# Performance work log

Hardware: AMD Instinct MI355X
Metric: run time of the kernel (lower is better)

The kernel has to match this reference:

```python
import jax, jax.numpy as jnp
import numpy as np

B, T, IN, H, OUT = 256, 100, 128, 1024, 35
BITS = 4
SLOPE = 25.0
THR_H = 1.0
THR_O = 1.0
BETA1, BETA2, BETA3, BETA4 = 0.9, 0.85, 0.8, 0.95


def fake_quant(w, w_min, w_max, bits=BITS):
    # FakeQuantize in training mode: STE -> forward value is quantized, grad passes through clamp
    levels = 2 ** bits
    scale = (w_max - w_min) / (levels - 1)
    wc = jnp.clip(w, w_min, w_max)
    q = jnp.round((wc - w_min) / scale) * scale + w_min
    return wc + jax.lax.stop_gradient(q - wc)


@jax.custom_vjp
def spike(x):
    # Heaviside forward, fast-sigmoid surrogate backward (snn.surrogate.fast_sigmoid)
    return (x > 0).astype(x.dtype)

def _spike_fwd(x):
    return (x > 0).astype(x.dtype), x

def _spike_bwd(x, g):
    return (g / (SLOPE * jnp.abs(x) + 1.0) ** 2,)

spike.defvjp(_spike_fwd, _spike_bwd)


def lif_step(cur, mem, beta, thr, reset_mechanism):
    # snntorch Leaky (reset_delay semantics): reset computed from previous mem, detached
    reset = jax.lax.stop_gradient((mem > thr).astype(cur.dtype))
    base = beta * mem + cur
    if reset_mechanism == "subtract":
        mem_new = base - reset * thr
    else:  # "zero"
        mem_new = base - reset * base
    spk = spike(mem_new - thr)
    return spk, mem_new


def setup_inputs() -> dict:
    key = jax.random.key(0)
    ks = jax.random.split(key, 5)
    x = jax.random.normal(ks[0], (B, T, IN), dtype=jnp.float32)
    # QuantLinear init: uniform(w_min, w_max); fc1 uses (-0.5, 0.5), others (0.001, 1.0)
    w1 = jax.random.uniform(ks[1], (H, IN), minval=-0.5, maxval=0.5, dtype=jnp.float32)
    w2 = jax.random.uniform(ks[2], (H, H), minval=0.001, maxval=1.0, dtype=jnp.float32)
    w3 = jax.random.uniform(ks[3], (H, H), minval=0.001, maxval=1.0, dtype=jnp.float32)
    w4 = jax.random.uniform(ks[4], (OUT, H), minval=0.001, maxval=1.0, dtype=jnp.float32)
    return {"x": x, "w1": w1, "w2": w2, "w3": w3, "w4": w4}


def reference(x, w1, w2, w3, w4):
    # hoist weight quantization out of the time loop (identical math each step)
    q1 = fake_quant(w1, -0.5, 0.5)
    q2 = fake_quant(w2, 0.001, 1.0)
    q3 = fake_quant(w3, 0.001, 1.0)
    q4 = fake_quant(w4, 0.001, 1.0)
    xs = jnp.transpose(x, (1, 0, 2)) / 15.0  # [T, B, IN]
    Bx = x.shape[0]

    def step(carry, xt):
        m1, m2, m3, m4 = carry
        s1, m1 = lif_step(xt @ q1.T, m1, BETA1, THR_H, "subtract")
        s2, m2 = lif_step(s1 @ q2.T, m2, BETA2, THR_H, "subtract")
        s3, m3 = lif_step(s2 @ q3.T, m3, BETA3, THR_H, "subtract")
        s4, m4 = lif_step(s3 @ q4.T, m4, BETA4, THR_O, "zero")
        return (m1, m2, m3, m4), (s1, s2, s3, s4, m4)

    init = (jnp.zeros((Bx, H), x.dtype), jnp.zeros((Bx, H), x.dtype),
            jnp.zeros((Bx, H), x.dtype), jnp.zeros((Bx, OUT), x.dtype))
    _, (spk1, spk2, spk3, spk4, mem4) = jax.lax.scan(step, init, xs)
    # stacked along time dim 0, matching torch.stack(dim=0)
    return spk1, spk2, spk3, spk4, mem4
```

## Files before the change

### kernel.cpp

```cpp
#include <hip/hip_runtime.h>
#include <stdint.h>

#define NB  256
#define NT  100
#define NIN 128
#define NH  1024
#define NOUT 35
#define NR  25600

#define O_SPK2 26214400ull
#define O_SPK3 52428800ull
#define O_SPK4 78643200ull
#define O_MEM4 79539200ull

#define WS_KBUF 0ull
#define WS_SPKB 52428800ull
#define WS_K2B  78643200ull
#define WS_K3B  79691776ull
#define WS_K4B  80740352ull
#define WS_Q1T  80871424ull
#define WS_N1   81395712ull
#define WS_N2   81498112ull
#define WS_N3   81600512ull

#define S2C ((float)((1.0 - 0.001) / 15.0))
#define S1C ((float)(1.0 / 15.0))

typedef int v4i __attribute__((ext_vector_type(4)));

__device__ __forceinline__ void async16(const void* g, void* l) {
  __builtin_amdgcn_global_load_lds((const __attribute__((address_space(1))) uint32_t*)g,
                                   (__attribute__((address_space(3))) uint32_t*)l, 16, 0, 0);
}

__device__ __forceinline__ uint8_t qk(float w) {
  float wc = fminf(fmaxf(w, 0.001f), 1.0f);
  return (uint8_t)(int)rintf((wc - 0.001f) / S2C);
}

__global__ void k_prep(const float* __restrict__ w1, const float* __restrict__ w2,
                       const float* __restrict__ w3, const float* __restrict__ w4,
                       uint8_t* __restrict__ ws)
{
  long long id = (long long)blockIdx.x * 256 + threadIdx.x;
  if (id < 1048576) { ws[WS_K2B + id] = qk(w2[id]); return; }
  id -= 1048576;
  if (id < 1048576) { ws[WS_K3B + id] = qk(w3[id]); return; }
  id -= 1048576;
  if (id < 131072) {
    int j = (int)(id >> 10), i = (int)(id & 1023);
    ws[WS_K4B + id] = (j < NOUT) ? qk(w4[(size_t)j * 1024 + i]) : (uint8_t)0;
    return;
  }
  id -= 131072;
  if (id < 131072) {
    int i = (int)(id >> 10), j = (int)(id & 1023);
    float wv = w1[(size_t)j * 128 + i];
    float wc = fminf(fmaxf(wv, -0.5f), 0.5f);
    float q = rintf((wc + 0.5f) / S1C) * S1C - 0.5f;
    ((float*)(ws + WS_Q1T))[id] = q;
    return;
  }
  id -= 131072;
  if (id < 76800) ((uint32_t*)(ws + WS_N1))[id] = 0;
}

__global__ __launch_bounds__(256) void k_cur1(const float* __restrict__ x,
                                              const uint8_t* __restrict__ ws,
                                              float* __restrict__ out)
{
  __shared__ float xsT[128 * 68];
  __shared__ float qch[16 * 256];
  const float* q1T = (const float*)(ws + WS_Q1T);
  const int tid = threadIdx.x;
  const int rb = blockIdx.x >> 2, cb = blockIdx.x & 3;
  const int t = rb >> 2, b0 = (rb & 3) * 64;
  const int jI = tid & 63, rI = tid >> 6;
  const int j4 = jI * 4, r16 = rI * 16;

  #pragma unroll
  for (int k = 0; k < 32; ++k) {
    int e = tid + k * 256;
    int r = e >> 7, i = e & 127;
    xsT[i * 68 + r] = x[((size_t)(b0 + r) * NT + t) * NIN + i] / 15.0f;
  }
  float acc[16][4];
  #pragma unroll
  for (int d = 0; d < 16; ++d) { acc[d][0]=0.f; acc[d][1]=0.f; acc[d][2]=0.f; acc[d][3]=0.f; }
  for (int ic = 0; ic < 8; ++ic) {
    __syncthreads();
    #pragma unroll
    for (int k = 0; k < 16; ++k) {
      int e = tid + k * 256;
      int ii = e >> 8, j = e & 255;
      qch[ii * 256 + j] = q1T[((size_t)(ic * 16 + ii) << 10) + cb * 256 + j];
    }
    __syncthreads();
    #pragma unroll
    for (int ii = 0; ii < 16; ++ii) {
      int i = ic * 16 + ii;
      const float4 q  = *(const float4*)&qch[ii * 256 + j4];
      const float4 xa = *(const float4*)&xsT[i * 68 + r16];
      const float4 xb = *(const float4*)&xsT[i * 68 + r16 + 4];
      const float4 xc = *(const float4*)&xsT[i * 68 + r16 + 8];
      const float4 xd = *(const float4*)&xsT[i * 68 + r16 + 12];
      float xr[16];
      xr[0]=xa.x; xr[1]=xa.y; xr[2]=xa.z; xr[3]=xa.w;
      xr[4]=xb.x; xr[5]=xb.y; xr[6]=xb.z; xr[7]=xb.w;
      xr[8]=xc.x; xr[9]=xc.y; xr[10]=xc.z; xr[11]=xc.w;
      xr[12]=xd.x; xr[13]=xd.y; xr[14]=xd.z; xr[15]=xd.w;
      #pragma unroll
      for (int d = 0; d < 16; ++d) {
        acc[d][0] = fmaf(xr[d], q.x, acc[d][0]);
        acc[d][1] = fmaf(xr[d], q.y, acc[d][1]);
        acc[d][2] = fmaf(xr[d], q.z, acc[d][2]);
        acc[d][3] = fmaf(xr[d], q.w, acc[d][3]);
      }
    }
  }
  #pragma unroll
  for (int d = 0; d < 16; ++d) {
    float4 v = make_float4(acc[d][0], acc[d][1], acc[d][2], acc[d][3]);
    *(float4*)&out[((size_t)rb * 64 + r16 + d) * 1024 + cb * 256 + j4] = v;
  }
}

__global__ __launch_bounds__(256) void k_scan1(uint8_t* __restrict__ ws, float* __restrict__ out)
{
  const int tid = threadIdx.x;
  const int b = blockIdx.x >> 2;
  const int j = (blockIdx.x & 3) * 256 + tid;
  uint8_t* spkb = ws + WS_SPKB;
  uint32_t* n1 = (uint32_t*)(ws + WS_N1);
  const size_t stride = (size_t)NB * NH;
  size_t idx = (size_t)b * NH + j;
  float m = 0.f;
  float c = out[idx];
  for (int t = 0; t < NT; ++t) {
    float cn = (t + 1 < NT) ? out[idx + stride] : 0.f;
    float rst = m > 1.0f ? 1.0f : 0.0f;
    m = fmaf(0.9f, m, c) - rst;
    bool sp = (m - 1.0f) > 0.0f;
    out[idx] = sp ? 1.0f : 0.0f;
    spkb[idx] = sp ? 1 : 0;
    unsigned long long bal = __ballot(sp);
    if ((tid & 63) == 0) atomicAdd((unsigned int*)&n1[t * NB + b], (unsigned)__popcll(bal));
    idx += stride; c = cn;
  }
}

__global__ __launch_bounds__(256) void k_gemm(const uint8_t* __restrict__ A,
                                              const uint8_t* __restrict__ Bm,
                                              uint16_t* __restrict__ C, int ncb)
{
  __shared__ uint8_t sA[16384];
  __shared__ uint8_t sB[16384];
  const int tid = threadIdx.x, lane = tid & 63, wave = tid >> 6;
  const int lm = lane & 15, lk = lane >> 4;
  const int rb = blockIdx.x, jb = blockIdx.y;
  const int mw = wave & 1, nw = wave >> 1;
  v4i acc[4][4];
  #pragma unroll
  for (int a = 0; a < 4; ++a)
    #pragma unroll
    for (int bb = 0; bb < 4; ++bb) { acc[a][bb][0]=0; acc[a][bb][1]=0; acc[a][bb][2]=0; acc[a][bb][3]=0; }

  for (int kk = 0; kk < 1024; kk += 128) {
    __syncthreads();
    #pragma unroll
    for (int q = 0; q < 8; ++q) {
      int cid = wave * 8 + q;
      if (cid < 16) {
        int kh = cid >> 3, cm = cid & 7;
        const uint8_t* g = A + (size_t)(rb * 128 + cm * 16 + lm) * 1024 + kk + kh * 64 + (lk << 4);
        async16(g, sA + cid * 1024);
      } else {
        int cb2 = cid - 16;
        int kh = cb2 >> 3, cn = cb2 & 7;
        const uint8_t* g = Bm + (size_t)(jb * 128 + cn * 16 + lm) * 1024 + kk + kh * 64 + (lk << 4);
        async16(g, sB + cb2 * 1024);
      }
    }
    __syncthreads();
    #pragma unroll
    for (int kh = 0; kh < 2; ++kh) {
      v4i av[4], bv[4];
      #pragma unroll
      for (int mi = 0; mi < 4; ++mi)
        av[mi] = *(const v4i*)(sA + (size_t)(kh * 8 + mw * 4 + mi) * 1024 + lane * 16);
      #pragma unroll
      for (int ni = 0; ni < 4; ++ni)
        bv[ni] = *(const v4i*)(sB + (size_t)(kh * 8 + nw * 4 + ni) * 1024 + lane * 16);
      #pragma unroll
      for (int mi = 0; mi < 4; ++mi)
        #pragma unroll
        for (int ni = 0; ni < 4; ++ni)
          acc[mi][ni] = __builtin_amdgcn_mfma_i32_16x16x64_i8(av[mi], bv[ni], acc[mi][ni], 0, 0, 0);
    }
  }
  const int rowb = rb * 128 + mw * 64;
  const int colb = jb * 128 + nw * 64;
  const int strideC = ncb * 128;
  #pragma unroll
  for (int mi = 0; mi < 4; ++mi)
    #pragma unroll
    for (int ni = 0; ni < 4; ++ni)
      #pragma unroll
      for (int r = 0; r < 4; ++r) {
        int row = rowb + mi * 16 + (lane >> 4) * 4 + r;
        int col = colb + ni * 16 + (lane & 15);
        C[(size_t)row * strideC + col] = (uint16_t)acc[mi][ni][r];
      }
}

__global__ __launch_bounds__(256) void k_scan23(const uint16_t* __restrict__ Kin,
                                                const uint32_t* __restrict__ nprev,
                                                uint32_t* __restrict__ nout,
                                                float beta,
                                                float* __restrict__ outB,
                                                uint8_t* __restrict__ spkb)
{
  const int tid = threadIdx.x;
  const int b = blockIdx.x >> 2;
  const int j = (blockIdx.x & 3) * 256 + tid;
  const size_t stride = (size_t)NB * NH;
  size_t idx = (size_t)b * NH + j;
  float m = 0.f;
  uint16_t kv = Kin[idx];
  for (int t = 0; t < NT; ++t) {
    uint16_t kn = (t + 1 < NT) ? Kin[idx + stride] : (uint16_t)0;
    float nb = 0.001f * (float)nprev[t * NB + b];
    float cur = fmaf(S2C, (float)kv, nb);
    float rst = m > 1.0f ? 1.0f : 0.0f;
    m = fmaf(beta, m, cur) - rst;
    bool sp = (m - 1.0f) > 0.0f;
    outB[idx] = sp ? 1.0f : 0.0f;
    spkb[idx] = sp ? 1 : 0;
    unsigned long long bal = __ballot(sp);
    if ((tid & 63) == 0) atomicAdd((unsigned int*)&nout[t * NB + b], (unsigned)__popcll(bal));
    idx += stride; kv = kn;
  }
}

__global__ __launch_bounds__(64) void k_scan4(const uint8_t* __restrict__ ws, float* __restrict__ out)
{
  const int b = blockIdx.x;
  const int j = threadIdx.x;
  const uint16_t* K4 = (const uint16_t*)(ws + WS_KBUF);
  const uint32_t* n3 = (const uint32_t*)(ws + WS_N3);
  size_t idx = (size_t)b * 128 + j;
  const size_t stride = (size_t)NB * 128;
  float m = 0.f;
  uint16_t kv = (j < NOUT) ? K4[idx] : (uint16_t)0;
  for (int t = 0; t < NT; ++t) {
    uint16_t kn = (t + 1 < NT && j < NOUT) ? K4[idx + stride] : (uint16_t)0;
    float cur = fmaf(S2C, (float)kv, 0.001f * (float)n3[t * NB + b]);
    float rst = m > 1.0f ? 1.0f : 0.0f;
    float bsv = fmaf(0.95f, m, cur);
    m = (rst > 0.0f) ? 0.0f : bsv;
    if (j < NOUT) {
      size_t rowO = ((size_t)t * NB + b) * NOUT + j;
      out[O_SPK4 + rowO] = ((m - 1.0f) > 0.0f) ? 1.0f : 0.0f;
      out[O_MEM4 + rowO] = m;
    }
    idx += stride; kv = kn;
  }
}

extern "C" void kernel_launch(void* const* d_in, const int* in_sizes, int n_in,
                              void* d_out, int out_size, void* d_ws, size_t ws_size,
                              hipStream_t stream)
{
  const float* x  = (const float*)d_in[0];
  const float* w1 = (const float*)d_in[1];
  const float* w2 = (const float*)d_in[2];
  const float* w3 = (const float*)d_in[3];
  const float* w4 = (const float*)d_in[4];
  float* out = (float*)d_out;
  uint8_t* ws = (uint8_t*)d_ws;

  uint16_t* KBUF = (uint16_t*)(ws + WS_KBUF);
  uint8_t*  SPKB = ws + WS_SPKB;
  uint32_t* N1 = (uint32_t*)(ws + WS_N1);
  uint32_t* N2 = (uint32_t*)(ws + WS_N2);
  uint32_t* N3 = (uint32_t*)(ws + WS_N3);

  hipLaunchKernelGGL(k_prep, dim3(9517), dim3(256), 0, stream, w1, w2, w3, w4, ws);
  hipLaunchKernelGGL(k_cur1, dim3(1600), dim3(256), 0, stream, x, ws, out);
  hipLaunchKernelGGL(k_scan1, dim3(1024), dim3(256), 0, stream, ws, out);
  hipLaunchKernelGGL(k_gemm, dim3(200, 8), dim3(256), 0, stream, SPKB, ws + WS_K2B, KBUF, 8);
  hipLaunchKernelGGL(k_scan23, dim3(1024), dim3(256), 0, stream, KBUF, N1, N2, 0.85f, out + O_SPK2, SPKB);
  hipLaunchKernelGGL(k_gemm, dim3(200, 8), dim3(256), 0, stream, SPKB, ws + WS_K3B, KBUF, 8);
  hipLaunchKernelGGL(k_scan23, dim3(1024), dim3(256), 0, stream, KBUF, N2, N3, 0.8f, out + O_SPK3, SPKB);
  hipLaunchKernelGGL(k_gemm, dim3(200, 1), dim3(256), 0, stream, SPKB, ws + WS_K4B, KBUF, 1);
  hipLaunchKernelGGL(k_scan4, dim3(256), dim3(64), 0, stream, ws, out);
}
```

Before: 747.2 us.

## Fuse per-layer GEMM with LIF time scan using per-batch tiles over time

Each layer's matmul and its time-recurrent LIF scan now run in one kernel. Blocks tile over (batch, 128 output columns), and the M dimension is the 100 timesteps padded to 112. The GEMM result stays in LDS and a single thread per column scans it over time. This removes the intermediate uint16 current buffer round trip through global memory and cuts the launch count. In exchange, only 128 threads per block do the serial scan, and padded rows add some wasted MFMA work.

```diff
diff --git a/kernel.cpp b/kernel.cpp
--- a/kernel.cpp
+++ b/kernel.cpp
@@ -6,22 +6,22 @@
 #define NIN 128
 #define NH  1024
 #define NOUT 35
-#define NR  25600
+#define MT  112
 
 #define O_SPK2 26214400ull
 #define O_SPK3 52428800ull
 #define O_SPK4 78643200ull
 #define O_MEM4 79539200ull
 
-#define WS_KBUF 0ull
-#define WS_SPKB 52428800ull
-#define WS_K2B  78643200ull
-#define WS_K3B  79691776ull
-#define WS_K4B  80740352ull
-#define WS_Q1T  80871424ull
-#define WS_N1   81395712ull
-#define WS_N2   81498112ull
-#define WS_N3   81600512ull
+#define WS_SPK0 0ull
+#define WS_SPK1 29360128ull
+#define WS_K2B  58720256ull
+#define WS_K3B  59768832ull
+#define WS_K4B  60817408ull
+#define WS_Q1T  60866560ull
+#define WS_N1   61390848ull
+#define WS_N2   61493248ull
+#define WS_N3   61595648ull
 
 #define S2C ((float)((1.0 - 0.001) / 15.0))
 #define S1C ((float)(1.0 / 15.0))
@@ -47,12 +47,12 @@
   id -= 1048576;
   if (id < 1048576) { ws[WS_K3B + id] = qk(w3[id]); return; }
   id -= 1048576;
-  if (id < 131072) {
+  if (id < 49152) {
     int j = (int)(id >> 10), i = (int)(id & 1023);
     ws[WS_K4B + id] = (j < NOUT) ? qk(w4[(size_t)j * 1024 + i]) : (uint8_t)0;
     return;
   }
-  id -= 131072;
+  id -= 49152;
   if (id < 131072) {
     int i = (int)(id >> 10), j = (int)(id & 1023);
     float wv = w1[(size_t)j * 128 + i];
@@ -65,205 +65,244 @@
   if (id < 76800) ((uint32_t*)(ws + WS_N1))[id] = 0;
 }
 
-__global__ __launch_bounds__(256) void k_cur1(const float* __restrict__ x,
-                                              const uint8_t* __restrict__ ws,
-                                              float* __restrict__ out)
-{
-  __shared__ float xsT[128 * 68];
-  __shared__ float qch[16 * 256];
+__global__ __launch_bounds__(256) void k_l1(const float* __restrict__ x,
+                                            uint8_t* __restrict__ ws,
+                                            float* __restrict__ out)
+{
+  __shared__ float lds[128 * 116 + 128 * 128];
+  float* xsT = lds;
+  float* qs  = lds + 128 * 116;
+  float* cbuf = lds;
   const float* q1T = (const float*)(ws + WS_Q1T);
+  uint8_t* spk0 = ws + WS_SPK0;
+  uint32_t* n1 = (uint32_t*)(ws + WS_N1);
+
+  const int b = blockIdx.x, jb = blockIdx.y;
   const int tid = threadIdx.x;
-  const int rb = blockIdx.x >> 2, cb = blockIdx.x & 3;
-  const int t = rb >> 2, b0 = (rb & 3) * 64;
-  const int jI = tid & 63, rI = tid >> 6;
-  const int j4 = jI * 4, r16 = rI * 16;
-
-  #pragma unroll
-  for (int k = 0; k < 32; ++k) {
-    int e = tid + k * 256;
-    int r = e >> 7, i = e & 127;
-    xsT[i * 68 + r] = x[((size_t)(b0 + r) * NT + t) * NIN + i] / 15.0f;
-  }
-  float acc[16][4];
-  #pragma unroll
-  for (int d = 0; d < 16; ++d) { acc[d][0]=0.f; acc[d][1]=0.f; acc[d][2]=0.f; acc[d][3]=0.f; }
-  for (int ic = 0; ic < 8; ++ic) {
-    __syncthreads();
-    #pragma unroll
-    for (int k = 0; k < 16; ++k) {
-      int e = tid + k * 256;
-      int ii = e >> 8, j = e & 255;
-      qch[ii * 256 + j] = q1T[((size_t)(ic * 16 + ii) << 10) + cb * 256 + j];
-    }
-    __syncthreads();
-    #pragma unroll
-    for (int ii = 0; ii < 16; ++ii) {
-      int i = ic * 16 + ii;
-      const float4 q  = *(const float4*)&qch[ii * 256 + j4];
-      const float4 xa = *(const float4*)&xsT[i * 68 + r16];
-      const float4 xb = *(const float4*)&xsT[i * 68 + r16 + 4];
-      const float4 xc = *(const float4*)&xsT[i * 68 + r16 + 8];
-      const float4 xd = *(const float4*)&xsT[i * 68 + r16 + 12];
-      float xr[16];
-      xr[0]=xa.x; xr[1]=xa.y; xr[2]=xa.z; xr[3]=xa.w;
-      xr[4]=xb.x; xr[5]=xb.y; xr[6]=xb.z; xr[7]=xb.w;
-      xr[8]=xc.x; xr[9]=xc.y; xr[10]=xc.z; xr[11]=xc.w;
-      xr[12]=xd.x; xr[13]=xd.y; xr[14]=xd.z; xr[15]=xd.w;
-      #pragma unroll
-      for (int d = 0; d < 16; ++d) {
-        acc[d][0] = fmaf(xr[d], q.x, acc[d][0]);
-        acc[d][1] = fmaf(xr[d], q.y, acc[d][1]);
-        acc[d][2] = fmaf(xr[d], q.z, acc[d][2]);
-        acc[d][3] = fmaf(xr[d], q.w, acc[d][3]);
-      }
-    }
-  }
-  #pragma unroll
-  for (int d = 0; d < 16; ++d) {
-    float4 v = make_float4(acc[d][0], acc[d][1], acc[d][2], acc[d][3]);
-    *(float4*)&out[((size_t)rb * 64 + r16 + d) * 1024 + cb * 256 + j4] = v;
-  }
-}
-
-__global__ __launch_bounds__(256) void k_scan1(uint8_t* __restrict__ ws, float* __restrict__ out)
-{
-  const int tid = threadIdx.x;
-  const int b = blockIdx.x >> 2;
-  const int j = (blockIdx.x & 3) * 256 + tid;
-  uint8_t* spkb = ws + WS_SPKB;
-  uint32_t* n1 = (uint32_t*)(ws + WS_N1);
-  const size_t stride = (size_t)NB * NH;
-  size_t idx = (size_t)b * NH + j;
-  float m = 0.f;
-  float c = out[idx];
-  for (int t = 0; t < NT; ++t) {
-    float cn = (t + 1 < NT) ? out[idx + stride] : 0.f;
-    float rst = m > 1.0f ? 1.0f : 0.0f;
-    m = fmaf(0.9f, m, c) - rst;
-    bool sp = (m - 1.0f) > 0.0f;
-    out[idx] = sp ? 1.0f : 0.0f;
-    spkb[idx] = sp ? 1 : 0;
-    unsigned long long bal = __ballot(sp);
-    if ((tid & 63) == 0) atomicAdd((unsigned int*)&n1[t * NB + b], (unsigned)__popcll(bal));
-    idx += stride; c = cn;
-  }
-}
-
-__global__ __launch_bounds__(256) void k_gemm(const uint8_t* __restrict__ A,
-                                              const uint8_t* __restrict__ Bm,
-                                              uint16_t* __restrict__ C, int ncb)
-{
-  __shared__ uint8_t sA[16384];
-  __shared__ uint8_t sB[16384];
+  const int ty = tid >> 4, tx = tid & 15;
+
+  #pragma unroll
+  for (int it = 0; it < 50; ++it) {
+    int e = tid + it * 256;
+    int t = e >> 7, i = e & 127;
+    xsT[i * 116 + t] = x[(size_t)b * 12800 + e] / 15.0f;
+  }
+  #pragma unroll
+  for (int it = 0; it < 32; ++it) {
+    int e4 = (tid + it * 256) * 4;
+    int i = e4 >> 7, j = e4 & 127;
+    *(float4*)&qs[i * 128 + j] = *(const float4*)&q1T[(size_t)i * 1024 + jb * 128 + j];
+  }
+  __syncthreads();
+
+  float acc[7][8];
+  #pragma unroll
+  for (int i = 0; i < 7; ++i)
+    #pragma unroll
+    for (int j = 0; j < 8; ++j) acc[i][j] = 0.f;
+
+  #pragma unroll 4
+  for (int k = 0; k < 128; ++k) {
+    float a[7], q[8];
+    #pragma unroll
+    for (int i = 0; i < 7; ++i) a[i] = xsT[k * 116 + ty + 16 * i];
+    #pragma unroll
+    for (int j = 0; j < 8; ++j) q[j] = qs[k * 128 + tx + 16 * j];
+    #pragma unroll
+    for (int i = 0; i < 7; ++i)
+      #pragma unroll
+      for (int j = 0; j < 8; ++j)
+        acc[i][j] = fmaf(a[i], q[j], acc[i][j]);
+  }
+  __syncthreads();
+  #pragma unroll
+  for (int i = 0; i < 7; ++i)
+    #pragma unroll
+    for (int j = 0; j < 8; ++j)
+      cbuf[(ty + 16 * i) * 132 + tx + 16 * j] = acc[i][j];
+  __syncthreads();
+
+  if (tid < 128) {
+    int j = tid;
+    float m = 0.f;
+    for (int t = 0; t < NT; ++t) {
+      float c = cbuf[t * 132 + j];
+      float rst = m > 1.0f ? 1.0f : 0.0f;
+      m = fmaf(0.9f, m, c) - rst;
+      bool sp = (m - 1.0f) > 0.0f;
+      out[((size_t)t * NB + b) * NH + jb * 128 + j] = sp ? 1.0f : 0.0f;
+      spk0[((size_t)b * MT + t) * 1024 + jb * 128 + j] = sp ? 1 : 0;
+      unsigned long long bal = __ballot(sp);
+      if ((tid & 63) == 0) atomicAdd((unsigned int*)&n1[t * NB + b], (unsigned)__popcll(bal));
+    }
+    for (int t = NT; t < MT; ++t)
+      spk0[((size_t)b * MT + t) * 1024 + jb * 128 + j] = 0;
+  }
+}
+
+__global__ __launch_bounds__(256) void k_l23(const uint8_t* __restrict__ Aspk,
+                                             const uint8_t* __restrict__ Bq,
+                                             const uint32_t* __restrict__ nprev,
+                                             uint32_t* __restrict__ nout,
+                                             float beta,
+                                             float* __restrict__ outF,
+                                             uint8_t* __restrict__ spkOut)
+{
+  __shared__ uint8_t lds[61440];
+  __shared__ uint32_t nbuf[112];
+  uint8_t* sA = lds;
+  uint8_t* sB = lds + 28672;
+  uint16_t* cbuf = (uint16_t*)lds;
+
+  const int b = blockIdx.x, jb = blockIdx.y;
   const int tid = threadIdx.x, lane = tid & 63, wave = tid >> 6;
   const int lm = lane & 15, lk = lane >> 4;
-  const int rb = blockIdx.x, jb = blockIdx.y;
-  const int mw = wave & 1, nw = wave >> 1;
-  v4i acc[4][4];
-  #pragma unroll
-  for (int a = 0; a < 4; ++a)
-    #pragma unroll
-    for (int bb = 0; bb < 4; ++bb) { acc[a][bb][0]=0; acc[a][bb][1]=0; acc[a][bb][2]=0; acc[a][bb][3]=0; }
-
-  for (int kk = 0; kk < 1024; kk += 128) {
+
+  if (tid < NT) nbuf[tid] = nprev[tid * NB + b];
+
+  const uint8_t* Ab = Aspk + (size_t)b * MT * 1024;
+  const uint8_t* Bb = Bq + (size_t)jb * 128 * 1024;
+
+  v4i acc[7][2];
+  #pragma unroll
+  for (int m = 0; m < 7; ++m)
+    #pragma unroll
+    for (int n = 0; n < 2; ++n) { acc[m][n][0]=0; acc[m][n][1]=0; acc[m][n][2]=0; acc[m][n][3]=0; }
+
+  for (int kk = 0; kk < 1024; kk += 256) {
     __syncthreads();
     #pragma unroll
-    for (int q = 0; q < 8; ++q) {
-      int cid = wave * 8 + q;
-      if (cid < 16) {
-        int kh = cid >> 3, cm = cid & 7;
-        const uint8_t* g = A + (size_t)(rb * 128 + cm * 16 + lm) * 1024 + kk + kh * 64 + (lk << 4);
-        async16(g, sA + cid * 1024);
-      } else {
-        int cb2 = cid - 16;
-        int kh = cb2 >> 3, cn = cb2 & 7;
-        const uint8_t* g = Bm + (size_t)(jb * 128 + cn * 16 + lm) * 1024 + kk + kh * 64 + (lk << 4);
-        async16(g, sB + cb2 * 1024);
+    for (int q = 0; q < 15; ++q) {
+      int cid = wave * 15 + q;
+      if (cid < 28) {
+        int mt = cid >> 2, ks = cid & 3;
+        async16(Ab + (size_t)(mt * 16 + lm) * 1024 + kk + ks * 64 + lk * 16, sA + cid * 1024);
+      } else if (cid < 60) {
+        int c2 = cid - 28, nt = c2 >> 2, ks = c2 & 3;
+        async16(Bb + (size_t)(nt * 16 + lm) * 1024 + kk + ks * 64 + lk * 16, sB + c2 * 1024);
       }
     }
     __syncthreads();
     #pragma unroll
-    for (int kh = 0; kh < 2; ++kh) {
-      v4i av[4], bv[4];
-      #pragma unroll
-      for (int mi = 0; mi < 4; ++mi)
-        av[mi] = *(const v4i*)(sA + (size_t)(kh * 8 + mw * 4 + mi) * 1024 + lane * 16);
-      #pragma unroll
-      for (int ni = 0; ni < 4; ++ni)
-        bv[ni] = *(const v4i*)(sB + (size_t)(kh * 8 + nw * 4 + ni) * 1024 + lane * 16);
-      #pragma unroll
-      for (int mi = 0; mi < 4; ++mi)
+    for (int ks = 0; ks < 4; ++ks) {
+      v4i bv0 = *(const v4i*)(sB + (size_t)((2 * wave) * 4 + ks) * 1024 + lane * 16);
+      v4i bv1 = *(const v4i*)(sB + (size_t)((2 * wave + 1) * 4 + ks) * 1024 + lane * 16);
+      #pragma unroll
+      for (int m = 0; m < 7; ++m) {
+        v4i av = *(const v4i*)(sA + (size_t)(m * 4 + ks) * 1024 + lane * 16);
+        acc[m][0] = __builtin_amdgcn_mfma_i32_16x16x64_i8(av, bv0, acc[m][0], 0, 0, 0);
+        acc[m][1] = __builtin_amdgcn_mfma_i32_16x16x64_i8(av, bv1, acc[m][1], 0, 0, 0);
+      }
+    }
+  }
+  __syncthreads();
+  #pragma unroll
+  for (int m = 0; m < 7; ++m)
+    #pragma unroll
+    for (int n = 0; n < 2; ++n)
+      #pragma unroll
+      for (int r = 0; r < 4; ++r) {
+        int row = m * 16 + lk * 4 + r;
+        int col = (2 * wave + n) * 16 + lm;
+        cbuf[row * 132 + col] = (uint16_t)acc[m][n][r];
+      }
+  __syncthreads();
+
+  if (tid < 128) {
+    int j = tid;
+    float m = 0.f;
+    for (int t = 0; t < NT; ++t) {
+      int kv = cbuf[t * 132 + j];
+      float cur = fmaf(S2C, (float)kv, 0.001f * (float)nbuf[t]);
+      float rst = m > 1.0f ? 1.0f : 0.0f;
+      m = fmaf(beta, m, cur) - rst;
+      bool sp = (m - 1.0f) > 0.0f;
+      outF[((size_t)t * NB + b) * NH + jb * 128 + j] = sp ? 1.0f : 0.0f;
+      spkOut[((size_t)b * MT + t) * 1024 + jb * 128 + j] = sp ? 1 : 0;
+      unsigned long long bal = __ballot(sp);
+      if ((tid & 63) == 0) atomicAdd((unsigned int*)&nout[t * NB + b], (unsigned)__popcll(bal));
+    }
+    for (int t = NT; t < MT; ++t)
+      spkOut[((size_t)b * MT + t) * 1024 + jb * 128 + j] = 0;
+  }
+}
+
+__global__ __launch_bounds__(256) void k_l4(const uint8_t* __restrict__ Aspk,
+                                            const uint8_t* __restrict__ ws,
+                                            float* __restrict__ out)
+{
+  __shared__ uint8_t lds[40960];
+  __shared__ uint32_t nbuf[112];
+  uint8_t* sA = lds;
+  uint8_t* sB = lds + 28672;
+  uint16_t* cbuf = (uint16_t*)lds;
+
+  const int b = blockIdx.x;
+  const int tid = threadIdx.x, lane = tid & 63, wave = tid >> 6;
+  const int lm = lane & 15, lk = lane >> 4;
+  const uint8_t* Bq = ws + WS_K4B;
+  const uint32_t* n3 = (const uint32_t*)(ws + WS_N3);
+
+  if (tid < NT) nbuf[tid] = n3[tid * NB + b];
+
+  const uint8_t* Ab = Aspk + (size_t)b * MT * 1024;
+
+  v4i acc[7];
+  #pragma unroll
+  for (int m = 0; m < 7; ++m) { acc[m][0]=0; acc[m][1]=0; acc[m][2]=0; acc[m][3]=0; }
+
+  for (int kk = 0; kk < 1024; kk += 256) {
+    __syncthreads();
+    #pragma unroll
+    for (int q = 0; q < 10; ++q) {
+      int cid = wave * 10 + q;
+      if (cid < 28) {
+        int mt = cid >> 2, ks = cid & 3;
+        async16(Ab + (size_t)(mt * 16 + lm) * 1024 + kk + ks * 64 + lk * 16, sA + cid * 1024);
+      } else if (cid < 40) {
+        int c2 = cid - 28, nt = c2 >> 2, ks = c2 & 3;
+        async16(Bq + (size_t)(nt * 16 + lm) * 1024 + kk + ks * 64 + lk * 16, sB + c2 * 1024);
+      }
+    }
+    __syncthreads();
+    if (wave < 3) {
+      #pragma unroll
+      for (int ks = 0; ks < 4; ++ks) {
+        v4i bv = *(const v4i*)(sB + (size_t)(wave * 4 + ks) * 1024 + lane * 16);
         #pragma unroll
-        for (int ni = 0; ni < 4; ++ni)
-          acc[mi][ni] = __builtin_amdgcn_mfma_i32_16x16x64_i8(av[mi], bv[ni], acc[mi][ni], 0, 0, 0);
-    }
-  }
-  const int rowb = rb * 128 + mw * 64;
-  const int colb = jb * 128 + nw * 64;
-  const int strideC = ncb * 128;
-  #pragma unroll
-  for (int mi = 0; mi < 4; ++mi)
-    #pragma unroll
-    for (int ni = 0; ni < 4; ++ni)
+        for (int m = 0; m < 7; ++m) {
+          v4i av = *(const v4i*)(sA + (size_t)(m * 4 + ks) * 1024 + lane * 16);
+          acc[m] = __builtin_amdgcn_mfma_i32_16x16x64_i8(av, bv, acc[m], 0, 0, 0);
+        }
+      }
+    }
+  }
+  __syncthreads();
+  if (wave < 3) {
+    #pragma unroll
+    for (int m = 0; m < 7; ++m)
       #pragma unroll
       for (int r = 0; r < 4; ++r) {
-        int row = rowb + mi * 16 + (lane >> 4) * 4 + r;
-        int col = colb + ni * 16 + (lane & 15);
-        C[(size_t)row * strideC + col] = (uint16_t)acc[mi][ni][r];
-      }
-}
-
-__global__ __launch_bounds__(256) void k_scan23(const uint16_t* __restrict__ Kin,
-                                                const uint32_t* __restrict__ nprev,
-                                                uint32_t* __restrict__ nout,
-                                                float beta,
-                                                float* __restrict__ outB,
-                                                uint8_t* __restrict__ spkb)
-{
-  const int tid = threadIdx.x;
-  const int b = blockIdx.x >> 2;
-  const int j = (blockIdx.x & 3) * 256 + tid;
-  const size_t stride = (size_t)NB * NH;
-  size_t idx = (size_t)b * NH + j;
-  float m = 0.f;
-  uint16_t kv = Kin[idx];
-  for (int t = 0; t < NT; ++t) {
-    uint16_t kn = (t + 1 < NT) ? Kin[idx + stride] : (uint16_t)0;
-    float nb = 0.001f * (float)nprev[t * NB + b];
-    float cur = fmaf(S2C, (float)kv, nb);
-    float rst = m > 1.0f ? 1.0f : 0.0f;
-    m = fmaf(beta, m, cur) - rst;
-    bool sp = (m - 1.0f) > 0.0f;
-    outB[idx] = sp ? 1.0f : 0.0f;
-    spkb[idx] = sp ? 1 : 0;
-    unsigned long long bal = __ballot(sp);
-    if ((tid & 63) == 0) atomicAdd((unsigned int*)&nout[t * NB + b], (unsigned)__popcll(bal));
-    idx += stride; kv = kn;
-  }
-}
-
-__global__ __launch_bounds__(64) void k_scan4(const uint8_t* __restrict__ ws, float* __restrict__ out)
-{
-  const int b = blockIdx.x;
-  const int j = threadIdx.x;
-  const uint16_t* K4 = (const uint16_t*)(ws + WS_KBUF);
-  const uint32_t* n3 = (const uint32_t*)(ws + WS_N3);
-  size_t idx = (size_t)b * 128 + j;
-  const size_t stride = (size_t)NB * 128;
-  float m = 0.f;
-  uint16_t kv = (j < NOUT) ? K4[idx] : (uint16_t)0;
-  for (int t = 0; t < NT; ++t) {
-    uint16_t kn = (t + 1 < NT && j < NOUT) ? K4[idx + stride] : (uint16_t)0;
-    float cur = fmaf(S2C, (float)kv, 0.001f * (float)n3[t * NB + b]);
-    float rst = m > 1.0f ? 1.0f : 0.0f;
-    float bsv = fmaf(0.95f, m, cur);
-    m = (rst > 0.0f) ? 0.0f : bsv;
-    if (j < NOUT) {
+        int row = m * 16 + lk * 4 + r;
+        int col = wave * 16 + lm;
+        cbuf[row * 52 + col] = (uint16_t)acc[m][r];
+      }
+  }
+  __syncthreads();
+
+  if (tid < NOUT) {
+    int j = tid;
+    float m = 0.f;
+    for (int t = 0; t < NT; ++t) {
+      int kv = cbuf[t * 52 + j];
+      float cur = fmaf(S2C, (float)kv, 0.001f * (float)nbuf[t]);
+      float rst = m > 1.0f ? 1.0f : 0.0f;
+      float bsv = fmaf(0.95f, m, cur);
+      m = (rst > 0.0f) ? 0.0f : bsv;
       size_t rowO = ((size_t)t * NB + b) * NOUT + j;
       out[O_SPK4 + rowO] = ((m - 1.0f) > 0.0f) ? 1.0f : 0.0f;
       out[O_MEM4 + rowO] = m;
     }
-    idx += stride; kv = kn;
   }
 }
 
@@ -279,19 +318,17 @@
   float* out = (float*)d_out;
   uint8_t* ws = (uint8_t*)d_ws;
 
-  uint16_t* KBUF = (uint16_t*)(ws + WS_KBUF);
-  uint8_t*  SPKB = ws + WS_SPKB;
+  uint8_t* SPK0 = ws + WS_SPK0;
+  uint8_t* SPK1 = ws + WS_SPK1;
   uint32_t* N1 = (uint32_t*)(ws + WS_N1);
   uint32_t* N2 = (uint32_t*)(ws + WS_N2);
   uint32_t* N3 = (uint32_t*)(ws + WS_N3);
 
-  hipLaunchKernelGGL(k_prep, dim3(9517), dim3(256), 0, stream, w1, w2, w3, w4, ws);
-  hipLaunchKernelGGL(k_cur1, dim3(1600), dim3(256), 0, stream, x, ws, out);
-  hipLaunchKernelGGL(k_scan1, dim3(1024), dim3(256), 0, stream, ws, out);
-  hipLaunchKernelGGL(k_gemm, dim3(200, 8), dim3(256), 0, stream, SPKB, ws + WS_K2B, KBUF, 8);
-  hipLaunchKernelGGL(k_scan23, dim3(1024), dim3(256), 0, stream, KBUF, N1, N2, 0.85f, out + O_SPK2, SPKB);
-  hipLaunchKernelGGL(k_gemm, dim3(200, 8), dim3(256), 0, stream, SPKB, ws + WS_K3B, KBUF, 8);
-  hipLaunchKernelGGL(k_scan23, dim3(1024), dim3(256), 0, stream, KBUF, N2, N3, 0.8f, out + O_SPK3, SPKB);
-  hipLaunchKernelGGL(k_gemm, dim3(200, 1), dim3(256), 0, stream, SPKB, ws + WS_K4B, KBUF, 1);
-  hipLaunchKernelGGL(k_scan4, dim3(256), dim3(64), 0, stream, ws, out);
-}
+  hipLaunchKernelGGL(k_prep, dim3(9196), dim3(256), 0, stream, w1, w2, w3, w4, ws);
+  hipLaunchKernelGGL(k_l1,  dim3(256, 8), dim3(256), 0, stream, x, ws, out);
+  hipLaunchKernelGGL(k_l23, dim3(256, 8), dim3(256), 0, stream,
+                     SPK0, ws + WS_K2B, N1, N2, 0.85f, out + O_SPK2, SPK1);
+  hipLaunchKernelGGL(k_l23, dim3(256, 8), dim3(256), 0, stream,
+                     SPK1, ws + WS_K3B, N2, N3, 0.8f, out + O_SPK3, SPK0);
+  hipLaunchKernelGGL(k_l4,  dim3(256), dim3(256), 0, stream, SPK0, ws, out);
+}
```

Result: slower. 838.2 us (+12.2%).
